# Kernel optimization log

Measured on AMD Instinct MI355X. Metric: run time of the kernel, lower is better.

## Reference

```python
import jax, jax.numpy as jnp
import numpy as np

NUM_HEADS = 8
BN_EPS = 1e-5
ATTN_EPS = 1e-6

def setup_inputs() -> dict:
    key = jax.random.key(0)
    N, E, D = 50000, 600000, 128
    ks = jax.random.split(key, 7)
    s = 1.0 / np.sqrt(D).astype(np.float32)
    return {
        'x': jax.random.normal(ks[0], (N, D), jnp.float32),
        'edge_attr': jax.random.normal(ks[1], (E, D), jnp.float32),
        'WQ': jax.random.normal(ks[2], (D, D), jnp.float32) * s,
        'WK': jax.random.normal(ks[3], (D, D), jnp.float32) * s,
        'WV': jax.random.normal(ks[4], (D, D), jnp.float32) * s,
        'WE': jax.random.normal(ks[5], (D, D), jnp.float32) * s,
        'bn_gamma': jnp.ones((D,), jnp.float32),
        'bn_beta': jnp.zeros((D,), jnp.float32),
        'edge_index': jax.random.randint(ks[6], (2, E), 0, N, dtype=jnp.int32),
    }

def reference(x, edge_attr, WQ, WK, WV, WE, bn_gamma, bn_beta, edge_index):
    N, D = x.shape
    H = NUM_HEADS
    dh = D // H  # head dim
    # Projections (no bias), split into heads: [N, H, dh]
    Q = (x @ WQ).reshape(N, H, dh)
    K = (x @ WK).reshape(N, H, dh)
    V = (x @ WV).reshape(N, H, dh)
    Eh = (edge_attr @ WE).reshape(-1, H, dh)  # [E, H, dh]
    src, dst = edge_index[0], edge_index[1]
    # Per-edge attention score modulated by edge features
    score = (K[src] * Q[dst]) / jnp.sqrt(jnp.float32(dh)) * Eh  # [E, H, dh]
    score = jnp.exp(jnp.clip(score.sum(-1, keepdims=True), -5.0, 5.0))  # [E, H, 1]
    msg = V[src] * score  # [E, H, dh]
    wV = jax.ops.segment_sum(msg, dst, num_segments=N)  # [N, H, dh]
    Z = jax.ops.segment_sum(score, dst, num_segments=N)  # [N, H, 1]
    h_attn = (wV / (Z + ATTN_EPS)).reshape(N, D)
    # Residual (dropout p=0 is identity) + BatchNorm1d (training statistics)
    h = x + h_attn
    mean = h.mean(axis=0)
    var = jnp.mean((h - mean) ** 2, axis=0)
    return (h - mean) * jax.lax.rsqrt(var + BN_EPS) * bn_gamma + bn_beta
```

## Files before the change

### kernel.cpp

```cpp
#include <hip/hip_runtime.h>
#include <math.h>


typedef __attribute__((ext_vector_type(8))) short short8;
typedef __attribute__((ext_vector_type(4))) float f32x4;

__device__ __forceinline__ unsigned short f2bf(float x) {
    unsigned int u = __float_as_uint(x);
    return (unsigned short)((u + 0x7FFFu + ((u >> 16) & 1u)) >> 16);
}

__global__ __launch_bounds__(128) void qkv_kernel(
    const float* __restrict__ x, const float* __restrict__ WQ,
    const float* __restrict__ WK, const float* __restrict__ WV,
    float* __restrict__ Q, float* __restrict__ K, float* __restrict__ V,
    int N)
{
    const int t = threadIdx.x;
    const int r0 = blockIdx.x * 8;
    __shared__ float xs[8][128];
#pragma unroll
    for (int r = 0; r < 8; ++r)
        xs[r][t] = (r0 + r < N) ? x[(size_t)(r0 + r) * 128 + t] : 0.f;
    __syncthreads();

    float aq[8] = {0}, ak[8] = {0}, av[8] = {0};
#pragma unroll 2
    for (int k4 = 0; k4 < 32; ++k4) {
        const float* wq = WQ + (size_t)(k4 * 4) * 128 + t;
        const float* wk = WK + (size_t)(k4 * 4) * 128 + t;
        const float* wv = WV + (size_t)(k4 * 4) * 128 + t;
        float q0 = wq[0], q1 = wq[128], q2 = wq[256], q3 = wq[384];
        float k0 = wk[0], k1 = wk[128], k2 = wk[256], k3 = wk[384];
        float v0 = wv[0], v1 = wv[128], v2 = wv[256], v3 = wv[384];
#pragma unroll
        for (int r = 0; r < 8; ++r) {
            float4 xv = *(const float4*)&xs[r][k4 * 4];
            aq[r] += xv.x * q0 + xv.y * q1 + xv.z * q2 + xv.w * q3;
            ak[r] += xv.x * k0 + xv.y * k1 + xv.z * k2 + xv.w * k3;
            av[r] += xv.x * v0 + xv.y * v1 + xv.z * v2 + xv.w * v3;
        }
    }
#pragma unroll
    for (int r = 0; r < 8; ++r) {
        if (r0 + r < N) {
            const size_t o = (size_t)(r0 + r) * 128 + t;
            Q[o] = aq[r]; K[o] = ak[r]; V[o] = av[r];
        }
    }
}

__global__ __launch_bounds__(256) void wet_kernel(
    const float* __restrict__ WE, unsigned short* __restrict__ WEt)
{
    const int i = blockIdx.x * 256 + threadIdx.x;
    const int n = i >> 7, k = i & 127;
    WEt[i] = f2bf(WE[k * 128 + n]);
}

#define ASTRIDE 136
#define ESTRIDE 132

__global__ __launch_bounds__(256, 4) void eh_score_kernel(
    const float* __restrict__ ea, const unsigned short* __restrict__ WEt,
    const float* __restrict__ Q, const float* __restrict__ K,
    const int* __restrict__ src, const int* __restrict__ dst,
    const int* __restrict__ eslot,
    float* __restrict__ score, int E)
{
    union Sm {
        unsigned short A[64 * ASTRIDE];
        float eh[64 * ESTRIDE];
    };
    __shared__ Sm sm;
    __shared__ int ssrc[64], sdst[64], sslot[64];
    const int t = threadIdx.x;
    const long e0 = (long)blockIdx.x * 64;

#pragma unroll
    for (int kk = 0; kk < 8; ++kk) {
        const int f = t + kk * 256;
        const int row = f >> 5, c4 = (f & 31) * 4;
        float4 v = make_float4(0.f, 0.f, 0.f, 0.f);
        if (e0 + row < E) v = *(const float4*)&ea[(size_t)(e0 + row) * 128 + c4];
        unsigned long long pk =  (unsigned long long)f2bf(v.x)
                              | ((unsigned long long)f2bf(v.y) << 16)
                              | ((unsigned long long)f2bf(v.z) << 32)
                              | ((unsigned long long)f2bf(v.w) << 48);
        *(unsigned long long*)&sm.A[row * ASTRIDE + c4] = pk;
    }
    if (t < 64) {
        const long e = e0 + t;
        ssrc[t]  = (e < E) ? src[e] : 0;
        sdst[t]  = (e < E) ? dst[e] : 0;
        sslot[t] = (e < E) ? eslot[e] : 0;
    }
    __syncthreads();

    const int w = t >> 6, l = t & 63;
    const int rb = (w >> 1) * 32, cb = (w & 1) * 64;
    const int lr = l & 15, quad = l >> 4;

    f32x4 acc[2][4];
#pragma unroll
    for (int i = 0; i < 2; ++i)
#pragma unroll
        for (int j = 0; j < 4; ++j) acc[i][j] = (f32x4){0.f, 0.f, 0.f, 0.f};

#pragma unroll
    for (int kb = 0; kb < 4; ++kb) {
        const int k0 = kb * 32 + quad * 8;
        short8 a0 = *(const short8*)&sm.A[(rb + lr) * ASTRIDE + k0];
        short8 a1 = *(const short8*)&sm.A[(rb + 16 + lr) * ASTRIDE + k0];
        short8 b0 = *(const short8*)&WEt[(cb + lr) * 128 + k0];
        short8 b1 = *(const short8*)&WEt[(cb + 16 + lr) * 128 + k0];
        short8 b2 = *(const short8*)&WEt[(cb + 32 + lr) * 128 + k0];
        short8 b3 = *(const short8*)&WEt[(cb + 48 + lr) * 128 + k0];
        acc[0][0] = __builtin_amdgcn_mfma_f32_16x16x32_bf16(a0, b0, acc[0][0], 0, 0, 0);
        acc[0][1] = __builtin_amdgcn_mfma_f32_16x16x32_bf16(a0, b1, acc[0][1], 0, 0, 0);
        acc[0][2] = __builtin_amdgcn_mfma_f32_16x16x32_bf16(a0, b2, acc[0][2], 0, 0, 0);
        acc[0][3] = __builtin_amdgcn_mfma_f32_16x16x32_bf16(a0, b3, acc[0][3], 0, 0, 0);
        acc[1][0] = __builtin_amdgcn_mfma_f32_16x16x32_bf16(a1, b0, acc[1][0], 0, 0, 0);
        acc[1][1] = __builtin_amdgcn_mfma_f32_16x16x32_bf16(a1, b1, acc[1][1], 0, 0, 0);
        acc[1][2] = __builtin_amdgcn_mfma_f32_16x16x32_bf16(a1, b2, acc[1][2], 0, 0, 0);
        acc[1][3] = __builtin_amdgcn_mfma_f32_16x16x32_bf16(a1, b3, acc[1][3], 0, 0, 0);
    }
    __syncthreads();

#pragma unroll
    for (int mi = 0; mi < 2; ++mi)
#pragma unroll
        for (int ni = 0; ni < 4; ++ni)
#pragma unroll
            for (int r = 0; r < 4; ++r)
                sm.eh[(rb + mi * 16 + quad * 4 + r) * ESTRIDE + cb + ni * 16 + lr] =
                    acc[mi][ni][r];
    __syncthreads();

#pragma unroll
    for (int pp = 0; pp < 2; ++pp) {
        const int p = t + pp * 256;
        const int e = p >> 3, h = p & 7;
        const long ge = e0 + e;
        if (ge < E) {
            const float* kp = K + (size_t)ssrc[e] * 128 + h * 16;
            const float* qp = Q + (size_t)sdst[e] * 128 + h * 16;
            const float* ep = &sm.eh[e * ESTRIDE + h * 16];
            float s = 0.f;
#pragma unroll
            for (int j = 0; j < 4; ++j) {
                float4 kv = *(const float4*)&kp[j * 4];
                float4 qv = *(const float4*)&qp[j * 4];
                float4 ev = *(const float4*)&ep[j * 4];
                s += kv.x * qv.x * ev.x + kv.y * qv.y * ev.y +
                     kv.z * qv.z * ev.z + kv.w * qv.w * ev.w;
            }
            score[(size_t)sslot[e] * 8 + h] = __expf(fminf(fmaxf(s * 0.25f, -5.f), 5.f));
        }
    }
}

__global__ __launch_bounds__(256) void hist_kernel(
    const int* __restrict__ dst, int* __restrict__ counts, int E)
{
    const int e = blockIdx.x * 256 + threadIdx.x;
    if (e < E) atomicAdd(&counts[dst[e]], 1);
}

__global__ __launch_bounds__(256) void scan_chunk_kernel(
    const int* __restrict__ in, int* __restrict__ excl,
    int* __restrict__ chunksums, int n)
{
    __shared__ int sm[256];
    const int t = threadIdx.x;
    const int i = blockIdx.x * 256 + t;
    const int v = (i < n) ? in[i] : 0;
    sm[t] = v;
    __syncthreads();
#pragma unroll
    for (int off = 1; off < 256; off <<= 1) {
        const int a = (t >= off) ? sm[t - off] : 0;
        __syncthreads();
        sm[t] += a;
        __syncthreads();
    }
    if (i < n) excl[i] = sm[t] - v;
    if (t == 255 && chunksums) chunksums[blockIdx.x] = sm[255];
}

__global__ __launch_bounds__(256) void add_offsets_kernel(
    int* __restrict__ excl, int* __restrict__ cursor,
    const int* __restrict__ chunkoff, int n)
{
    const int i = blockIdx.x * 256 + threadIdx.x;
    if (i < n) {
        const int v = excl[i] + chunkoff[blockIdx.x];
        excl[i] = v;
        cursor[i] = v;
    }
}

__global__ __launch_bounds__(256) void fill_sort_kernel(
    const int* __restrict__ src, const int* __restrict__ dst,
    int* __restrict__ cursor, int* __restrict__ eslot,
    int* __restrict__ srcs, int E)
{
    const int e = blockIdx.x * 256 + threadIdx.x;
    if (e < E) {
        const int slot = atomicAdd(&cursor[dst[e]], 1);
        eslot[e] = slot;
        srcs[slot] = src[e];
    }
}

__global__ __launch_bounds__(256) void aggregate_kernel(
    const float* __restrict__ V, const float* __restrict__ score,
    const int* __restrict__ srcs,
    const int* __restrict__ seg_start, const int* __restrict__ counts,
    const float* __restrict__ x, float* __restrict__ out,
    float* __restrict__ sums, int N)
{
    const int t = threadIdx.x;
    const int w = t >> 6, lane = t & 63;
    const int ha = lane >> 4, hb = 4 + (lane >> 4);
    float s1a = 0.f, s1b = 0.f, s2a = 0.f, s2b = 0.f;

    for (int node = blockIdx.x * 4 + w; node < N; node += gridDim.x * 4) {
        const int beg = seg_start[node];
        const int cnt = counts[node];
        float acc0 = 0.f, acc1 = 0.f, za = 0.f, zb = 0.f;
        if (cnt > 0) {
            int sA = srcs[beg];
            float saA = score[(size_t)beg * 8 + ha];
            float sbA = score[(size_t)beg * 8 + hb];
            const float* vA = V + (size_t)sA * 128;
            float vA0 = vA[lane], vA1 = vA[lane + 64];
            for (int j = 1; j < cnt; ++j) {
                const int sB = srcs[beg + j];
                const float saB = score[(size_t)(beg + j) * 8 + ha];
                const float sbB = score[(size_t)(beg + j) * 8 + hb];
                const float* vB = V + (size_t)sB * 128;
                const float vB0 = vB[lane], vB1 = vB[lane + 64];
                acc0 += saA * vA0; za += saA;
                acc1 += sbA * vA1; zb += sbA;
                saA = saB; sbA = sbB; vA0 = vB0; vA1 = vB1;
            }
            acc0 += saA * vA0; za += saA;
            acc1 += sbA * vA1; zb += sbA;
        }
        const size_t o = (size_t)node * 128 + lane;
        const float hv0 = x[o] + acc0 / (za + 1e-6f);
        const float hv1 = x[o + 64] + acc1 / (zb + 1e-6f);
        out[o] = hv0;
        out[o + 64] = hv1;
        s1a += hv0; s1b += hv1;
        s2a += hv0 * hv0; s2b += hv1 * hv1;
    }

    __shared__ float red[4][128];
    red[w][lane] = s1a; red[w][lane + 64] = s1b;
    __syncthreads();
    if (t < 128) atomicAdd(&sums[t], red[0][t] + red[1][t] + red[2][t] + red[3][t]);
    __syncthreads();
    red[w][lane] = s2a; red[w][lane + 64] = s2b;
    __syncthreads();
    if (t < 128) atomicAdd(&sums[128 + t], red[0][t] + red[1][t] + red[2][t] + red[3][t]);
}

__global__ void bn_scale_kernel(
    const float* __restrict__ sums,
    const float* __restrict__ gamma, const float* __restrict__ beta,
    float* __restrict__ sb, int N)
{
    const int c = threadIdx.x;
    const float invN = 1.0f / (float)N;
    const float mean = sums[c] * invN;
    const float var = sums[128 + c] * invN - mean * mean;
    const float sc = gamma[c] * rsqrtf(var + 1e-5f);
    sb[c] = sc;
    sb[128 + c] = beta[c] - mean * sc;
}

__global__ __launch_bounds__(256) void bn_apply_kernel(
    float* hw, const float* __restrict__ sb, size_t total)
{
    __shared__ float ssb[256];
    ssb[threadIdx.x] = sb[threadIdx.x];
    __syncthreads();
    const size_t n4 = total / 4;
    float4* h4 = (float4*)hw;
    for (size_t i = (size_t)blockIdx.x * blockDim.x + threadIdx.x; i < n4;
         i += (size_t)gridDim.x * blockDim.x) {
        const int c4 = (int)(i & 31) * 4;
        float4 v = h4[i];
        v.x = v.x * ssb[c4 + 0] + ssb[128 + c4 + 0];
        v.y = v.y * ssb[c4 + 1] + ssb[128 + c4 + 1];
        v.z = v.z * ssb[c4 + 2] + ssb[128 + c4 + 2];
        v.w = v.w * ssb[c4 + 3] + ssb[128 + c4 + 3];
        h4[i] = v;
    }
}

extern "C" void kernel_launch(void* const* d_in, const int* in_sizes, int n_in,
                              void* d_out, int out_size, void* d_ws, size_t ws_size,
                              hipStream_t stream)
{
    const float* x         = (const float*)d_in[0];
    const float* edge_attr = (const float*)d_in[1];
    const float* WQ        = (const float*)d_in[2];
    const float* WK        = (const float*)d_in[3];
    const float* WV        = (const float*)d_in[4];
    const float* WE        = (const float*)d_in[5];
    const float* gamma     = (const float*)d_in[6];
    const float* beta      = (const float*)d_in[7];
    const int*   eidx      = (const int*)d_in[8];

    const int N = in_sizes[0] / 128;
    const int E = in_sizes[8] / 2;
    const int* src = eidx;
    const int* dst = eidx + E;

    float* ws = (float*)d_ws;
    const size_t NB = (size_t)N * 128;
    float* Q     = ws;
    float* K     = ws + NB;
    float* V     = ws + 2 * NB;
    float* score = ws + 3 * NB;
    float* sums  = score + (size_t)E * 8;
    float* sb    = sums + 256;
    unsigned short* WEt = (unsigned short*)(sb + 256);
    int* counts    = (int*)(WEt + 128 * 128);
    int* seg_start = counts + N;
    int* cursor    = seg_start + N;
    int* chunksums = cursor + N;
    int* chunkoff  = chunksums + 256;
    int* eslot     = chunkoff + 256;
    int* srcs      = eslot + E;
    float* out = (float*)d_out;

    const int nch = (N + 255) / 256;

    hipMemsetAsync(counts, 0, (size_t)N * sizeof(int), stream);
    hipMemsetAsync(sums, 0, 256 * sizeof(float), stream);

    qkv_kernel<<<(N + 7) / 8, 128, 0, stream>>>(x, WQ, WK, WV, Q, K, V, N);
    wet_kernel<<<64, 256, 0, stream>>>(WE, WEt);
    hist_kernel<<<(E + 255) / 256, 256, 0, stream>>>(dst, counts, E);
    scan_chunk_kernel<<<nch, 256, 0, stream>>>(counts, seg_start, chunksums, N);
    scan_chunk_kernel<<<1, 256, 0, stream>>>(chunksums, chunkoff, nullptr, nch);
    add_offsets_kernel<<<nch, 256, 0, stream>>>(seg_start, cursor, chunkoff, N);
    fill_sort_kernel<<<(E + 255) / 256, 256, 0, stream>>>(src, dst, cursor, eslot,
                                                          srcs, E);
    eh_score_kernel<<<(E + 63) / 64, 256, 0, stream>>>(edge_attr, WEt, Q, K, src, dst,
                                                       eslot, score, E);
    aggregate_kernel<<<3200, 256, 0, stream>>>(V, score, srcs, seg_start, counts,
                                               x, out, sums, N);
    bn_scale_kernel<<<1, 128, 0, stream>>>(sums, gamma, beta, sb, N);
    bn_apply_kernel<<<2048, 256, 0, stream>>>(out, sb, NB);
}
```

Baseline: 851.1 us.

## Compute edge projection transposed in registers, removing shared-memory staging in score kernel

The edge-feature projection is restructured so each wave computes Eh^T for 16 edges: WE^T rows become the A operand and the edge features, loaded straight from global memory into B fragments, become the B operand. The MFMA output layout then matches the per-lane K/Q reads, and per-head dot products are reduced with lane shuffles. This removes all LDS staging, the eh spill, and the syncthreads, and raises the occupancy hint to 5. In exchange, edge features are loaded with strided per-lane accesses instead of coalesced block loads, and each wave reads the full WEt.

```diff
diff --git a/kernel.cpp b/kernel.cpp
--- a/kernel.cpp
+++ b/kernel.cpp
@@ -58,105 +58,76 @@
     WEt[i] = f2bf(WE[k * 128 + n]);
 }
 
-#define ASTRIDE 136
-#define ESTRIDE 132
-
-__global__ __launch_bounds__(256, 4) void eh_score_kernel(
+__global__ __launch_bounds__(256, 5) void eh_score_kernel(
     const float* __restrict__ ea, const unsigned short* __restrict__ WEt,
     const float* __restrict__ Q, const float* __restrict__ K,
     const int* __restrict__ src, const int* __restrict__ dst,
     const int* __restrict__ eslot,
     float* __restrict__ score, int E)
 {
-    union Sm {
-        unsigned short A[64 * ASTRIDE];
-        float eh[64 * ESTRIDE];
-    };
-    __shared__ Sm sm;
-    __shared__ int ssrc[64], sdst[64], sslot[64];
     const int t = threadIdx.x;
-    const long e0 = (long)blockIdx.x * 64;
-
-#pragma unroll
-    for (int kk = 0; kk < 8; ++kk) {
-        const int f = t + kk * 256;
-        const int row = f >> 5, c4 = (f & 31) * 4;
-        float4 v = make_float4(0.f, 0.f, 0.f, 0.f);
-        if (e0 + row < E) v = *(const float4*)&ea[(size_t)(e0 + row) * 128 + c4];
-        unsigned long long pk =  (unsigned long long)f2bf(v.x)
-                              | ((unsigned long long)f2bf(v.y) << 16)
-                              | ((unsigned long long)f2bf(v.z) << 32)
-                              | ((unsigned long long)f2bf(v.w) << 48);
-        *(unsigned long long*)&sm.A[row * ASTRIDE + c4] = pk;
-    }
-    if (t < 64) {
-        const long e = e0 + t;
-        ssrc[t]  = (e < E) ? src[e] : 0;
-        sdst[t]  = (e < E) ? dst[e] : 0;
-        sslot[t] = (e < E) ? eslot[e] : 0;
-    }
-    __syncthreads();
-
     const int w = t >> 6, l = t & 63;
-    const int rb = (w >> 1) * 32, cb = (w & 1) * 64;
     const int lr = l & 15, quad = l >> 4;
-
-    f32x4 acc[2][4];
-#pragma unroll
-    for (int i = 0; i < 2; ++i)
-#pragma unroll
-        for (int j = 0; j < 4; ++j) acc[i][j] = (f32x4){0.f, 0.f, 0.f, 0.f};
+    const long e = (long)blockIdx.x * 64 + w * 16 + lr;
+    const bool valid = (e < E);
+    const long es = valid ? e : 0;
+
+    const int s_i  = src[es];
+    const int d_i  = dst[es];
+    const int slot = eslot[es];
+
+    short8 bfrag[4];
+#pragma unroll
+    for (int kb = 0; kb < 4; ++kb) {
+        const float* ap = ea + (size_t)es * 128 + kb * 32 + quad * 8;
+        float4 v0 = *(const float4*)ap;
+        float4 v1 = *(const float4*)(ap + 4);
+        short8 b;
+        b[0] = (short)f2bf(v0.x); b[1] = (short)f2bf(v0.y);
+        b[2] = (short)f2bf(v0.z); b[3] = (short)f2bf(v0.w);
+        b[4] = (short)f2bf(v1.x); b[5] = (short)f2bf(v1.y);
+        b[6] = (short)f2bf(v1.z); b[7] = (short)f2bf(v1.w);
+        bfrag[kb] = b;
+    }
+
+    f32x4 acc[8];
+#pragma unroll
+    for (int h = 0; h < 8; ++h) acc[h] = (f32x4){0.f, 0.f, 0.f, 0.f};
 
 #pragma unroll
     for (int kb = 0; kb < 4; ++kb) {
         const int k0 = kb * 32 + quad * 8;
-        short8 a0 = *(const short8*)&sm.A[(rb + lr) * ASTRIDE + k0];
-        short8 a1 = *(const short8*)&sm.A[(rb + 16 + lr) * ASTRIDE + k0];
-        short8 b0 = *(const short8*)&WEt[(cb + lr) * 128 + k0];
-        short8 b1 = *(const short8*)&WEt[(cb + 16 + lr) * 128 + k0];
-        short8 b2 = *(const short8*)&WEt[(cb + 32 + lr) * 128 + k0];
-        short8 b3 = *(const short8*)&WEt[(cb + 48 + lr) * 128 + k0];
-        acc[0][0] = __builtin_amdgcn_mfma_f32_16x16x32_bf16(a0, b0, acc[0][0], 0, 0, 0);
-        acc[0][1] = __builtin_amdgcn_mfma_f32_16x16x32_bf16(a0, b1, acc[0][1], 0, 0, 0);
-        acc[0][2] = __builtin_amdgcn_mfma_f32_16x16x32_bf16(a0, b2, acc[0][2], 0, 0, 0);
-        acc[0][3] = __builtin_amdgcn_mfma_f32_16x16x32_bf16(a0, b3, acc[0][3], 0, 0, 0);
-        acc[1][0] = __builtin_amdgcn_mfma_f32_16x16x32_bf16(a1, b0, acc[1][0], 0, 0, 0);
-        acc[1][1] = __builtin_amdgcn_mfma_f32_16x16x32_bf16(a1, b1, acc[1][1], 0, 0, 0);
-        acc[1][2] = __builtin_amdgcn_mfma_f32_16x16x32_bf16(a1, b2, acc[1][2], 0, 0, 0);
-        acc[1][3] = __builtin_amdgcn_mfma_f32_16x16x32_bf16(a1, b3, acc[1][3], 0, 0, 0);
-    }
-    __syncthreads();
-
-#pragma unroll
-    for (int mi = 0; mi < 2; ++mi)
-#pragma unroll
-        for (int ni = 0; ni < 4; ++ni)
-#pragma unroll
-            for (int r = 0; r < 4; ++r)
-                sm.eh[(rb + mi * 16 + quad * 4 + r) * ESTRIDE + cb + ni * 16 + lr] =
-                    acc[mi][ni][r];
-    __syncthreads();
-
-#pragma unroll
-    for (int pp = 0; pp < 2; ++pp) {
-        const int p = t + pp * 256;
-        const int e = p >> 3, h = p & 7;
-        const long ge = e0 + e;
-        if (ge < E) {
-            const float* kp = K + (size_t)ssrc[e] * 128 + h * 16;
-            const float* qp = Q + (size_t)sdst[e] * 128 + h * 16;
-            const float* ep = &sm.eh[e * ESTRIDE + h * 16];
-            float s = 0.f;
-#pragma unroll
-            for (int j = 0; j < 4; ++j) {
-                float4 kv = *(const float4*)&kp[j * 4];
-                float4 qv = *(const float4*)&qp[j * 4];
-                float4 ev = *(const float4*)&ep[j * 4];
-                s += kv.x * qv.x * ev.x + kv.y * qv.y * ev.y +
-                     kv.z * qv.z * ev.z + kv.w * qv.w * ev.w;
-            }
-            score[(size_t)sslot[e] * 8 + h] = __expf(fminf(fmaxf(s * 0.25f, -5.f), 5.f));
+#pragma unroll
+        for (int h = 0; h < 8; ++h) {
+            short8 afrag = *(const short8*)&WEt[(h * 16 + lr) * 128 + k0];
+            acc[h] = __builtin_amdgcn_mfma_f32_16x16x32_bf16(afrag, bfrag[kb],
+                                                             acc[h], 0, 0, 0);
         }
+    }
+
+    const float* kp = K + (size_t)s_i * 128 + quad * 4;
+    const float* qp = Q + (size_t)d_i * 128 + quad * 4;
+    float part[8];
+#pragma unroll
+    for (int h = 0; h < 8; ++h) {
+        float4 kv = *(const float4*)(kp + h * 16);
+        float4 qv = *(const float4*)(qp + h * 16);
+        part[h] = acc[h][0] * kv.x * qv.x + acc[h][1] * kv.y * qv.y +
+                  acc[h][2] * kv.z * qv.z + acc[h][3] * kv.w * qv.w;
+    }
+#pragma unroll
+    for (int h = 0; h < 8; ++h) {
+        part[h] += __shfl_xor(part[h], 16);
+        part[h] += __shfl_xor(part[h], 32);
+    }
+    if (valid && quad < 2) {
+        const int hb = quad * 4;
+        float4 o;
+        o.x = __expf(fminf(fmaxf(part[hb + 0] * 0.25f, -5.f), 5.f));
+        o.y = __expf(fminf(fmaxf(part[hb + 1] * 0.25f, -5.f), 5.f));
+        o.z = __expf(fminf(fmaxf(part[hb + 2] * 0.25f, -5.f), 5.f));
+        o.w = __expf(fminf(fmaxf(part[hb + 3] * 0.25f, -5.f), 5.f));
+        *(float4*)&score[(size_t)slot * 8 + hb] = o;
     }
 }
 
```

After: 902.4 us. 6.0% more time.
